# Kernel tuning notes

Hardware: AMD Instinct MI355X
Metric: run time of the kernel (lower is better)

The kernel has to match this reference:

```python
import jax, jax.numpy as jnp
import numpy as np

DIM = 128
B, LQ, LK = 8, 2048, 2048


def setup_inputs() -> dict:
    key = jax.random.key(0)
    k1, k2, k3 = jax.random.split(key, 3)
    output = jax.random.normal(k1, (B, LQ, DIM), dtype=jnp.float32)
    context = jax.random.normal(k2, (B, LK, DIM), dtype=jnp.float32)
    mask = jax.random.randint(k3, (B, LQ, LK), 0, 2).astype(jnp.bool_)
    return {"output": output, "context": context, "mask": mask}


def reference(output, context, mask):
    temperature = jnp.asarray(np.power(DIM, 0.5), dtype=output.dtype)
    # scores: [B, Lq, Lk]
    attn = jnp.einsum('bqd,bkd->bqk', output, context) / temperature
    attn = jnp.where(mask, -jnp.inf, attn)
    out_attn = jax.nn.log_softmax(attn, axis=-1)
    p = jax.nn.softmax(attn, axis=-1)
    # dropout is identity in eval/reference mode
    out = jnp.einsum('bqk,bkd->bqd', p, context)
    return (out, out_attn)
```

## Files before the change

### kernel.cpp

```cpp
#include <hip/hip_runtime.h>
#include <cstdint>


#define DIMV 128
constexpr int BB = 8;
constexpr int LQ = 2048;
constexpr int LK = 2048;
constexpr float QSCALE = 0.08838834764831843f;

typedef _Float16 half8 __attribute__((ext_vector_type(8)));
typedef _Float16 half4v __attribute__((ext_vector_type(4)));
typedef float float4v __attribute__((ext_vector_type(4)));

__global__ __launch_bounds__(256) void prep_kernel(const float* __restrict__ q,
                                                   const float* __restrict__ ctx,
                                                   _Float16* __restrict__ Qf,
                                                   _Float16* __restrict__ Kf,
                                                   _Float16* __restrict__ Vf) {
    __shared__ float tile[32][132];
    const int tid  = threadIdx.x;
    const int mode = blockIdx.x >> 9;
    const int t    = blockIdx.x & 511;
    const int b    = t >> 6;
    const int r0   = (t & 63) * 32;
    const float4* s4 = (const float4*)((mode == 0 ? q : ctx) + ((size_t)b * 2048 + r0) * DIMV);
    for (int v = 0; v < 4; v++) {
        int off = tid + v * 256;
        float4 f = s4[off];
        int row = off >> 5, c4 = (off & 31) * 4;
        tile[row][c4 + 0] = f.x; tile[row][c4 + 1] = f.y;
        tile[row][c4 + 2] = f.z; tile[row][c4 + 3] = f.w;
    }
    __syncthreads();
    if (mode < 2) {
        const float qs = (mode == 0) ? QSCALE : 1.0f;
        _Float16* dst = (mode == 0 ? Qf : Kf) + (size_t)b * (2048 * DIMV);
        for (int c = 0; c < 2; c++) {
            int chunk = tid + c * 256;
            int t2 = chunk >> 8, kk = (chunk >> 6) & 3, lane = chunk & 63;
            int quad = lane >> 4, l16 = lane & 15;
            int r = t2 * 16 + l16, d0 = kk * 32 + quad * 8;
            half8 h;
            for (int e = 0; e < 8; e++) h[e] = (_Float16)(tile[r][d0 + e] * qs);
            size_t tl = (size_t)(r0 >> 4) + t2;
            *(half8*)(dst + ((tl * 4 + kk) * 64 + lane) * 8) = h;
        }
    } else {
        _Float16* dst = Vf + (size_t)b * (2048 * DIMV);
        const int kt0 = r0 >> 4;
        for (int c = 0; c < 2; c++) {
            int chunk = tid + c * 256;
            int ktl = chunk >> 8, dp = (chunk >> 6) & 3, ln = chunk & 63;
            int qd = ln >> 4, s16 = ln & 15;
            half8 h;
            for (int e = 0; e < 4; e++) {
                h[e]     = (_Float16)tile[ktl * 16 + qd * 4 + e][(2 * dp) * 16 + s16];
                h[e + 4] = (_Float16)tile[ktl * 16 + qd * 4 + e][(2 * dp + 1) * 16 + s16];
            }
            *(half8*)(dst + ((((size_t)(kt0 + ktl)) * 4 + dp) * 64 + ln) * 8) = h;
        }
    }
}

__global__ __launch_bounds__(512, 1)
void attn_kernel(const unsigned char* __restrict__ mask,
                 const _Float16* __restrict__ Qf, const _Float16* __restrict__ Kf,
                 const _Float16* __restrict__ Vf,
                 float* __restrict__ out, float* __restrict__ out_attn) {
    __shared__ __attribute__((aligned(16))) _Float16 STG[2][16384];
    __shared__ __attribute__((aligned(16))) float pvsum[64][132];
    __shared__ float redm[8][32], redl[8][32], swf[8][32];
    __shared__ float mcl64[64], rls64[64];

    const int tid  = threadIdx.x;
    const int wave = tid >> 6;
    const int lane = tid & 63;
    const int l16  = lane & 15;
    const int quad = lane >> 4;
    const int p    = wave & 3;
    const int qg   = wave >> 2;

    const int b   = blockIdx.x & 7;
    const int qt4 = blockIdx.x >> 3;
    const int q0  = qt4 * 64;

    const _Float16* Qb = Qf + (size_t)b * (2048 * DIMV);
    const _Float16* Kb = Kf + (size_t)b * (2048 * DIMV);
    const _Float16* Vb = Vf + (size_t)b * (2048 * DIMV);

    half8 qfrag[2][4];
#pragma unroll
    for (int sub = 0; sub < 2; sub++) {
        const size_t tq = (size_t)qt4 * 4 + qg * 2 + sub;
#pragma unroll
        for (int kk = 0; kk < 4; kk++)
            qfrag[sub][kk] = *(const half8*)(Qb + ((tq * 4 + kk) * 64 + lane) * 8);
    }

    const unsigned char* mrow0 = mask + ((size_t)b * LQ + q0 + qg * 32 + l16) * LK + p * 16 + quad * 4;

    const float NEGINF = -__builtin_inff();
    float m0r = -1e30f, m1r = -1e30f;
    float l0r = 0.f, l1r = 0.f;
    float4v oacc[2][8];
#pragma unroll
    for (int sub = 0; sub < 2; sub++)
#pragma unroll
        for (int dt = 0; dt < 8; dt++) oacc[sub][dt] = (float4v){0.f, 0.f, 0.f, 0.f};

    const _Float16* gsb = (wave < 4) ? Kb : Vb;
    const int wt = wave & 3;
    const unsigned dsto = ((wave < 4) ? 0u : 8192u) + (unsigned)wt * 2048;

    {
        const _Float16* src = gsb + (size_t)(0 * 4 + wt) * 2048 + lane * 8;
        float4 r4[4];
#pragma unroll
        for (int c = 0; c < 4; c++) r4[c] = *(const float4*)(src + c * 512);
        _Float16* d = &STG[0][dsto];
#pragma unroll
        for (int c = 0; c < 4; c++) *(float4*)(d + c * 512 + lane * 8) = r4[c];
    }
    __syncthreads();

    for (int i = 0; i < 32; ++i) {
        const int cur = i & 1, nxt = cur ^ 1;
        const bool more = (i + 1 < 32);
        float4 nr4[4];
        if (more) {
            const _Float16* src = gsb + (size_t)(4 * (i + 1) + wt) * 2048 + lane * 8;
#pragma unroll
            for (int c = 0; c < 4; c++) nr4[c] = *(const float4*)(src + c * 512);
        }

        const _Float16* kt = &STG[cur][p * 2048];
        const _Float16* vt = &STG[cur][8192 + p * 2048];
        half8 kf[4], vv[4];
#pragma unroll
        for (int kk = 0; kk < 4; kk++) kf[kk] = *(const half8*)(kt + kk * 512 + lane * 8);
#pragma unroll
        for (int dp = 0; dp < 4; dp++) vv[dp] = *(const half8*)(vt + dp * 512 + lane * 8);

#pragma unroll
        for (int sub = 0; sub < 2; sub++) {
            float4v st = (float4v){0.f, 0.f, 0.f, 0.f};
#pragma unroll
            for (int kk = 0; kk < 4; kk++)
                st = __builtin_amdgcn_mfma_f32_16x16x32_f16(kf[kk], qfrag[sub][kk], st, 0, 0, 0);
            const uint32_t mv = *(const uint32_t*)(mrow0 + (size_t)sub * 16 * LK + (size_t)i * 64);
            float& m = sub ? m1r : m0r;
            float& l = sub ? l1r : l0r;
            float sv[4];
#pragma unroll
            for (int r = 0; r < 4; r++) {
                float v = st[r];
                if ((mv >> (8 * r)) & 0xffu) v = NEGINF;
                sv[r] = v;
            }
            float tmax = fmaxf(fmaxf(sv[0], sv[1]), fmaxf(sv[2], sv[3]));
            tmax = fmaxf(tmax, __shfl_xor(tmax, 16));
            tmax = fmaxf(tmax, __shfl_xor(tmax, 32));
            const bool upd = tmax > m + 3.0f;
            if (__any(upd)) {
                const float mnew = upd ? tmax : m;
                const float sc = __expf(m - mnew);
                float scr[4];
#pragma unroll
                for (int r = 0; r < 4; r++) scr[r] = __shfl(sc, quad * 4 + r);
                l *= sc;
#pragma unroll
                for (int dt = 0; dt < 8; dt++)
#pragma unroll
                    for (int r = 0; r < 4; r++) oacc[sub][dt][r] *= scr[r];
                m = mnew;
            }
            half4v pa;
            float psum = 0.f;
#pragma unroll
            for (int r = 0; r < 4; r++) {
                const float pp = __expf(sv[r] - m);
                psum += pp;
                pa[r] = (_Float16)pp;
            }
            psum += __shfl_xor(psum, 16);
            psum += __shfl_xor(psum, 32);
            l += psum;
#pragma unroll
            for (int dp = 0; dp < 4; dp++) {
                half4v vlo = __builtin_shufflevector(vv[dp], vv[dp], 0, 1, 2, 3);
                half4v vhi = __builtin_shufflevector(vv[dp], vv[dp], 4, 5, 6, 7);
                oacc[sub][2 * dp]     = __builtin_amdgcn_mfma_f32_16x16x16f16(pa, vlo, oacc[sub][2 * dp],     0, 0, 0);
                oacc[sub][2 * dp + 1] = __builtin_amdgcn_mfma_f32_16x16x16f16(pa, vhi, oacc[sub][2 * dp + 1], 0, 0, 0);
            }
        }

        if (more) {
            _Float16* d = &STG[nxt][dsto];
#pragma unroll
            for (int c = 0; c < 4; c++) *(float4*)(d + c * 512 + lane * 8) = nr4[c];
        }
        __syncthreads();
    }

    if (quad == 0) {
        redm[wave][l16]      = m0r;  redm[wave][16 + l16] = m1r;
        redl[wave][l16]      = l0r;  redl[wave][16 + l16] = l1r;
    }
    float4 pre2[2];
    {
        const int t0 = wave >> 2, kkw = wave & 3;
        pre2[0] = *(const float4*)(Kb + (size_t)(t0)     * 2048 + kkw * 512 + lane * 8);
        pre2[1] = *(const float4*)(Kb + (size_t)(t0 + 2) * 2048 + kkw * 512 + lane * 8);
    }
    __syncthreads();
    if (tid < 64) {
        const int qg2 = tid >> 5, r32 = tid & 31;
        float mm[4], ll[4];
#pragma unroll
        for (int pp = 0; pp < 4; pp++) { mm[pp] = redm[qg2 * 4 + pp][r32]; ll[pp] = redl[qg2 * 4 + pp][r32]; }
        const float M = fmaxf(fmaxf(mm[0], mm[1]), fmaxf(mm[2], mm[3]));
        float L = 0.f;
#pragma unroll
        for (int pp = 0; pp < 4; pp++) {
            const float e = __expf(mm[pp] - M);
            swf[qg2 * 4 + pp][r32] = e;
            L += e * ll[pp];
        }
        mcl64[tid] = M + __logf(L);
        rls64[tid] = 1.0f / L;
    }
    __syncthreads();

    for (int rnd = 0; rnd < 4; ++rnd) {
        if (p == rnd) {
#pragma unroll
            for (int sub = 0; sub < 2; sub++)
#pragma unroll
                for (int r = 0; r < 4; r++) {
                    const int row = qg * 32 + sub * 16 + quad * 4 + r;
                    const float sc = swf[wave][sub * 16 + quad * 4 + r];
#pragma unroll
                    for (int dt = 0; dt < 8; dt++) {
                        const float v = oacc[sub][dt][r] * sc;
                        if (rnd == 0) pvsum[row][dt * 16 + l16] = v;
                        else          pvsum[row][dt * 16 + l16] += v;
                    }
                }
        }
        __syncthreads();
    }

    {
        const int row = tid >> 3;
        const int c0  = (tid & 7) * 16;
        const float rcl = rls64[row];
        float* op = out + ((size_t)b * LQ + q0 + row) * DIMV + c0;
#pragma unroll
        for (int h = 0; h < 4; h++) {
            float4v a = *(const float4v*)&pvsum[row][c0 + h * 4];
            float4v v;
#pragma unroll
            for (int j = 0; j < 4; j++) v[j] = a[j] * rcl;
            *(float4v*)(op + h * 4) = v;
        }
    }

    {
        const int t0 = wave >> 2, kkw = wave & 3;
        *(float4*)(&STG[0][(t0)     * 2048 + kkw * 512] + lane * 8) = pre2[0];
        *(float4*)(&STG[0][(t0 + 2) * 2048 + kkw * 512] + lane * 8) = pre2[1];
    }
    __syncthreads();

    const float mc0 = mcl64[qg * 32 + l16];
    const float mc1 = mcl64[qg * 32 + 16 + l16];
    float* oa0 = out_attn + ((size_t)b * LQ + q0 + qg * 32 + l16) * LK + p * 16 + quad * 4;
    for (int i = 0; i < 32; ++i) {
        const int cur = i & 1, nxt = cur ^ 1;
        const bool more = (i + 1 < 32);
        float4 n2[2];
        if (more) {
            const int t0 = wave >> 2, kkw = wave & 3;
            n2[0] = *(const float4*)(Kb + (size_t)(4 * (i + 1) + t0)     * 2048 + kkw * 512 + lane * 8);
            n2[1] = *(const float4*)(Kb + (size_t)(4 * (i + 1) + t0 + 2) * 2048 + kkw * 512 + lane * 8);
        }
        const _Float16* kt = &STG[cur][p * 2048];
        half8 kf[4];
#pragma unroll
        for (int kk = 0; kk < 4; kk++) kf[kk] = *(const half8*)(kt + kk * 512 + lane * 8);
#pragma unroll
        for (int sub = 0; sub < 2; sub++) {
            float4v st = (float4v){0.f, 0.f, 0.f, 0.f};
#pragma unroll
            for (int kk = 0; kk < 4; kk++)
                st = __builtin_amdgcn_mfma_f32_16x16x32_f16(kf[kk], qfrag[sub][kk], st, 0, 0, 0);
            const uint32_t mv = *(const uint32_t*)(mrow0 + (size_t)sub * 16 * LK + (size_t)i * 64);
            const float mc = sub ? mc1 : mc0;
            float4v o;
#pragma unroll
            for (int r = 0; r < 4; r++) {
                float lp = st[r] - mc;
                if ((mv >> (8 * r)) & 0xffu) lp = -1.0e30f;
                o[r] = fmaxf(lp, -1.0e30f);
            }
            *(float4v*)(oa0 + (size_t)sub * 16 * LK + (size_t)i * 64) = o;
        }
        if (more) {
            const int t0 = wave >> 2, kkw = wave & 3;
            *(float4*)(&STG[nxt][(t0)     * 2048 + kkw * 512] + lane * 8) = n2[0];
            *(float4*)(&STG[nxt][(t0 + 2) * 2048 + kkw * 512] + lane * 8) = n2[1];
        }
        __syncthreads();
    }
}

extern "C" void kernel_launch(void* const* d_in, const int* in_sizes, int n_in,
                              void* d_out, int out_size, void* d_ws, size_t ws_size,
                              hipStream_t stream) {
    const float* q_f32 = (const float*)d_in[0];
    const float* c_f32 = (const float*)d_in[1];
    const unsigned char* mask = (const unsigned char*)d_in[2];

    float* out      = (float*)d_out;
    float* out_attn = out + (size_t)BB * LQ * DIMV;

    _Float16* Qf = (_Float16*)d_ws;
    _Float16* Kf = Qf + (size_t)BB * LQ * DIMV;
    _Float16* Vf = Kf + (size_t)BB * LK * DIMV;

    prep_kernel<<<1536, 256, 0, stream>>>(q_f32, c_f32, Qf, Kf, Vf);
    attn_kernel<<<BB * (LQ / 64), 512, 0, stream>>>(mask, Qf, Kf, Vf, out, out_attn);
}
```

Baseline: 304.0 us.

## Drop LDS staging; each wave streams its own key strip into registers

The attention kernel moves from 512-thread blocks of 64 queries to 256-thread blocks of 32 queries. Each wave now owns a contiguous quarter of the keys and loads its K/V fragments and mask words straight from global memory into double-buffered registers, so the shared-memory staging buffers and the per-iteration __syncthreads are gone. MFMA sections are wrapped in s_setprio and a sched_barrier, and the row-sum reduction is moved after the PV MFMAs. The intent is to remove barrier stalls and LDS traffic and to allow two blocks per CU. In exchange, K/V are read from global or L2 by more blocks, and register pressure rises.

```diff
diff --git a/kernel.cpp b/kernel.cpp
--- a/kernel.cpp
+++ b/kernel.cpp
@@ -62,27 +62,24 @@
     }
 }
 
-__global__ __launch_bounds__(512, 1)
+__global__ __launch_bounds__(256, 2)
 void attn_kernel(const unsigned char* __restrict__ mask,
                  const _Float16* __restrict__ Qf, const _Float16* __restrict__ Kf,
                  const _Float16* __restrict__ Vf,
                  float* __restrict__ out, float* __restrict__ out_attn) {
-    __shared__ __attribute__((aligned(16))) _Float16 STG[2][16384];
-    __shared__ __attribute__((aligned(16))) float pvsum[64][132];
-    __shared__ float redm[8][32], redl[8][32], swf[8][32];
-    __shared__ float mcl64[64], rls64[64];
+    __shared__ __attribute__((aligned(16))) float pvsum[32][132];
+    __shared__ float redm[4][32], redl[4][32], swf[4][32];
+    __shared__ float mcl32[32], rls32[32];
 
     const int tid  = threadIdx.x;
     const int wave = tid >> 6;
     const int lane = tid & 63;
     const int l16  = lane & 15;
     const int quad = lane >> 4;
-    const int p    = wave & 3;
-    const int qg   = wave >> 2;
-
-    const int b   = blockIdx.x & 7;
-    const int qt4 = blockIdx.x >> 3;
-    const int q0  = qt4 * 64;
+
+    const int b  = blockIdx.x & 7;
+    const int qg = blockIdx.x >> 3;
+    const int q0 = qg * 32;
 
     const _Float16* Qb = Qf + (size_t)b * (2048 * DIMV);
     const _Float16* Kb = Kf + (size_t)b * (2048 * DIMV);
@@ -91,13 +88,16 @@
     half8 qfrag[2][4];
 #pragma unroll
     for (int sub = 0; sub < 2; sub++) {
-        const size_t tq = (size_t)qt4 * 4 + qg * 2 + sub;
+        const size_t tq = (size_t)qg * 2 + sub;
 #pragma unroll
         for (int kk = 0; kk < 4; kk++)
             qfrag[sub][kk] = *(const half8*)(Qb + ((tq * 4 + kk) * 64 + lane) * 8);
     }
 
-    const unsigned char* mrow0 = mask + ((size_t)b * LQ + q0 + qg * 32 + l16) * LK + p * 16 + quad * 4;
+    const unsigned char* mrow0 = mask + ((size_t)b * LQ + q0 + l16) * LK + wave * 512 + quad * 4;
+
+    const _Float16* kstrip = Kb + (size_t)wave * 32 * 2048;
+    const _Float16* vstrip = Vb + (size_t)wave * 32 * 2048;
 
     const float NEGINF = -__builtin_inff();
     float m0r = -1e30f, m1r = -1e30f;
@@ -108,46 +108,43 @@
 #pragma unroll
         for (int dt = 0; dt < 8; dt++) oacc[sub][dt] = (float4v){0.f, 0.f, 0.f, 0.f};
 
-    const _Float16* gsb = (wave < 4) ? Kb : Vb;
-    const int wt = wave & 3;
-    const unsigned dsto = ((wave < 4) ? 0u : 8192u) + (unsigned)wt * 2048;
-
+    half8 kfb[2][4], vvb[2][4];
+    uint32_t mvb[2][2];
     {
-        const _Float16* src = gsb + (size_t)(0 * 4 + wt) * 2048 + lane * 8;
-        float4 r4[4];
-#pragma unroll
-        for (int c = 0; c < 4; c++) r4[c] = *(const float4*)(src + c * 512);
-        _Float16* d = &STG[0][dsto];
-#pragma unroll
-        for (int c = 0; c < 4; c++) *(float4*)(d + c * 512 + lane * 8) = r4[c];
-    }
-    __syncthreads();
-
-    for (int i = 0; i < 32; ++i) {
-        const int cur = i & 1, nxt = cur ^ 1;
-        const bool more = (i + 1 < 32);
-        float4 nr4[4];
-        if (more) {
-            const _Float16* src = gsb + (size_t)(4 * (i + 1) + wt) * 2048 + lane * 8;
-#pragma unroll
-            for (int c = 0; c < 4; c++) nr4[c] = *(const float4*)(src + c * 512);
-        }
-
-        const _Float16* kt = &STG[cur][p * 2048];
-        const _Float16* vt = &STG[cur][8192 + p * 2048];
-        half8 kf[4], vv[4];
-#pragma unroll
-        for (int kk = 0; kk < 4; kk++) kf[kk] = *(const half8*)(kt + kk * 512 + lane * 8);
-#pragma unroll
-        for (int dp = 0; dp < 4; dp++) vv[dp] = *(const half8*)(vt + dp * 512 + lane * 8);
+#pragma unroll
+        for (int kk = 0; kk < 4; kk++) kfb[0][kk] = *(const half8*)(kstrip + (kk * 64 + lane) * 8);
+#pragma unroll
+        for (int dp = 0; dp < 4; dp++) vvb[0][dp] = *(const half8*)(vstrip + (dp * 64 + lane) * 8);
+#pragma unroll
+        for (int s = 0; s < 2; s++) mvb[0][s] = *(const uint32_t*)(mrow0 + (size_t)s * 16 * LK);
+    }
+
+#pragma unroll 2
+    for (int ct = 0; ct < 32; ++ct) {
+        const int cur = ct & 1, nxt = cur ^ 1;
+        const int cn  = (ct + 1) & 31;
+        {
+            const _Float16* kp = kstrip + (size_t)cn * 2048;
+            const _Float16* vp = vstrip + (size_t)cn * 2048;
+#pragma unroll
+            for (int kk = 0; kk < 4; kk++) kfb[nxt][kk] = *(const half8*)(kp + (kk * 64 + lane) * 8);
+#pragma unroll
+            for (int dp = 0; dp < 4; dp++) vvb[nxt][dp] = *(const half8*)(vp + (dp * 64 + lane) * 8);
+#pragma unroll
+            for (int s = 0; s < 2; s++)
+                mvb[nxt][s] = *(const uint32_t*)(mrow0 + (size_t)s * 16 * LK + cn * 16);
+        }
+        __builtin_amdgcn_sched_barrier(0);
 
 #pragma unroll
         for (int sub = 0; sub < 2; sub++) {
             float4v st = (float4v){0.f, 0.f, 0.f, 0.f};
+            __builtin_amdgcn_s_setprio(1);
 #pragma unroll
             for (int kk = 0; kk < 4; kk++)
-                st = __builtin_amdgcn_mfma_f32_16x16x32_f16(kf[kk], qfrag[sub][kk], st, 0, 0, 0);
-            const uint32_t mv = *(const uint32_t*)(mrow0 + (size_t)sub * 16 * LK + (size_t)i * 64);
+                st = __builtin_amdgcn_mfma_f32_16x16x32_f16(kfb[cur][kk], qfrag[sub][kk], st, 0, 0, 0);
+            __builtin_amdgcn_s_setprio(0);
+            const uint32_t mv = mvb[cur][sub];
             float& m = sub ? m1r : m0r;
             float& l = sub ? l1r : l0r;
             float sv[4];
@@ -175,70 +172,64 @@
                 m = mnew;
             }
             half4v pa;
-            float psum = 0.f;
+            float pp[4];
 #pragma unroll
             for (int r = 0; r < 4; r++) {
-                const float pp = __expf(sv[r] - m);
-                psum += pp;
-                pa[r] = (_Float16)pp;
-            }
+                pp[r] = __expf(sv[r] - m);
+                pa[r] = (_Float16)pp[r];
+            }
+            __builtin_amdgcn_s_setprio(1);
+#pragma unroll
+            for (int dp = 0; dp < 4; dp++) {
+                half4v vlo = __builtin_shufflevector(vvb[cur][dp], vvb[cur][dp], 0, 1, 2, 3);
+                half4v vhi = __builtin_shufflevector(vvb[cur][dp], vvb[cur][dp], 4, 5, 6, 7);
+                oacc[sub][2 * dp]     = __builtin_amdgcn_mfma_f32_16x16x16f16(pa, vlo, oacc[sub][2 * dp],     0, 0, 0);
+                oacc[sub][2 * dp + 1] = __builtin_amdgcn_mfma_f32_16x16x16f16(pa, vhi, oacc[sub][2 * dp + 1], 0, 0, 0);
+            }
+            __builtin_amdgcn_s_setprio(0);
+            float psum = (pp[0] + pp[1]) + (pp[2] + pp[3]);
             psum += __shfl_xor(psum, 16);
             psum += __shfl_xor(psum, 32);
             l += psum;
-#pragma unroll
-            for (int dp = 0; dp < 4; dp++) {
-                half4v vlo = __builtin_shufflevector(vv[dp], vv[dp], 0, 1, 2, 3);
-                half4v vhi = __builtin_shufflevector(vv[dp], vv[dp], 4, 5, 6, 7);
-                oacc[sub][2 * dp]     = __builtin_amdgcn_mfma_f32_16x16x16f16(pa, vlo, oacc[sub][2 * dp],     0, 0, 0);
-                oacc[sub][2 * dp + 1] = __builtin_amdgcn_mfma_f32_16x16x16f16(pa, vhi, oacc[sub][2 * dp + 1], 0, 0, 0);
-            }
-        }
-
-        if (more) {
-            _Float16* d = &STG[nxt][dsto];
-#pragma unroll
-            for (int c = 0; c < 4; c++) *(float4*)(d + c * 512 + lane * 8) = nr4[c];
-        }
-        __syncthreads();
+        }
     }
 
     if (quad == 0) {
         redm[wave][l16]      = m0r;  redm[wave][16 + l16] = m1r;
         redl[wave][l16]      = l0r;  redl[wave][16 + l16] = l1r;
     }
-    float4 pre2[2];
-    {
-        const int t0 = wave >> 2, kkw = wave & 3;
-        pre2[0] = *(const float4*)(Kb + (size_t)(t0)     * 2048 + kkw * 512 + lane * 8);
-        pre2[1] = *(const float4*)(Kb + (size_t)(t0 + 2) * 2048 + kkw * 512 + lane * 8);
-    }
+    half8 kf2[2][4];
+    uint32_t mv2[2][2];
+#pragma unroll
+    for (int kk = 0; kk < 4; kk++) kf2[0][kk] = *(const half8*)(kstrip + (kk * 64 + lane) * 8);
+#pragma unroll
+    for (int s = 0; s < 2; s++) mv2[0][s] = *(const uint32_t*)(mrow0 + (size_t)s * 16 * LK);
     __syncthreads();
-    if (tid < 64) {
-        const int qg2 = tid >> 5, r32 = tid & 31;
+    if (tid < 32) {
         float mm[4], ll[4];
 #pragma unroll
-        for (int pp = 0; pp < 4; pp++) { mm[pp] = redm[qg2 * 4 + pp][r32]; ll[pp] = redl[qg2 * 4 + pp][r32]; }
+        for (int p = 0; p < 4; p++) { mm[p] = redm[p][tid]; ll[p] = redl[p][tid]; }
         const float M = fmaxf(fmaxf(mm[0], mm[1]), fmaxf(mm[2], mm[3]));
         float L = 0.f;
 #pragma unroll
-        for (int pp = 0; pp < 4; pp++) {
-            const float e = __expf(mm[pp] - M);
-            swf[qg2 * 4 + pp][r32] = e;
-            L += e * ll[pp];
-        }
-        mcl64[tid] = M + __logf(L);
-        rls64[tid] = 1.0f / L;
+        for (int p = 0; p < 4; p++) {
+            const float e = __expf(mm[p] - M);
+            swf[p][tid] = e;
+            L += e * ll[p];
+        }
+        mcl32[tid] = M + __logf(L);
+        rls32[tid] = 1.0f / L;
     }
     __syncthreads();
 
     for (int rnd = 0; rnd < 4; ++rnd) {
-        if (p == rnd) {
+        if (wave == rnd) {
 #pragma unroll
             for (int sub = 0; sub < 2; sub++)
 #pragma unroll
                 for (int r = 0; r < 4; r++) {
-                    const int row = qg * 32 + sub * 16 + quad * 4 + r;
-                    const float sc = swf[wave][sub * 16 + quad * 4 + r];
+                    const int row = sub * 16 + quad * 4 + r;
+                    const float sc = swf[wave][row];
 #pragma unroll
                     for (int dt = 0; dt < 8; dt++) {
                         const float v = oacc[sub][dt][r] * sc;
@@ -253,7 +244,7 @@
     {
         const int row = tid >> 3;
         const int c0  = (tid & 7) * 16;
-        const float rcl = rls64[row];
+        const float rcl = rls32[row];
         float* op = out + ((size_t)b * LQ + q0 + row) * DIMV + c0;
 #pragma unroll
         for (int h = 0; h < 4; h++) {
@@ -265,36 +256,32 @@
         }
     }
 
-    {
-        const int t0 = wave >> 2, kkw = wave & 3;
-        *(float4*)(&STG[0][(t0)     * 2048 + kkw * 512] + lane * 8) = pre2[0];
-        *(float4*)(&STG[0][(t0 + 2) * 2048 + kkw * 512] + lane * 8) = pre2[1];
-    }
-    __syncthreads();
-
-    const float mc0 = mcl64[qg * 32 + l16];
-    const float mc1 = mcl64[qg * 32 + 16 + l16];
-    float* oa0 = out_attn + ((size_t)b * LQ + q0 + qg * 32 + l16) * LK + p * 16 + quad * 4;
-    for (int i = 0; i < 32; ++i) {
-        const int cur = i & 1, nxt = cur ^ 1;
-        const bool more = (i + 1 < 32);
-        float4 n2[2];
-        if (more) {
-            const int t0 = wave >> 2, kkw = wave & 3;
-            n2[0] = *(const float4*)(Kb + (size_t)(4 * (i + 1) + t0)     * 2048 + kkw * 512 + lane * 8);
-            n2[1] = *(const float4*)(Kb + (size_t)(4 * (i + 1) + t0 + 2) * 2048 + kkw * 512 + lane * 8);
-        }
-        const _Float16* kt = &STG[cur][p * 2048];
-        half8 kf[4];
-#pragma unroll
-        for (int kk = 0; kk < 4; kk++) kf[kk] = *(const half8*)(kt + kk * 512 + lane * 8);
+    const float mc0 = mcl32[l16];
+    const float mc1 = mcl32[16 + l16];
+    float* oa0 = out_attn + ((size_t)b * LQ + q0 + l16) * LK + wave * 512 + quad * 4;
+#pragma unroll 2
+    for (int ct = 0; ct < 32; ++ct) {
+        const int cur = ct & 1, nxt = cur ^ 1;
+        const int cn  = (ct + 1) & 31;
+        {
+            const _Float16* kp = kstrip + (size_t)cn * 2048;
+#pragma unroll
+            for (int kk = 0; kk < 4; kk++) kf2[nxt][kk] = *(const half8*)(kp + (kk * 64 + lane) * 8);
+#pragma unroll
+            for (int s = 0; s < 2; s++)
+                mv2[nxt][s] = *(const uint32_t*)(mrow0 + (size_t)s * 16 * LK + cn * 16);
+        }
+        __builtin_amdgcn_sched_barrier(0);
+
 #pragma unroll
         for (int sub = 0; sub < 2; sub++) {
             float4v st = (float4v){0.f, 0.f, 0.f, 0.f};
+            __builtin_amdgcn_s_setprio(1);
 #pragma unroll
             for (int kk = 0; kk < 4; kk++)
-                st = __builtin_amdgcn_mfma_f32_16x16x32_f16(kf[kk], qfrag[sub][kk], st, 0, 0, 0);
-            const uint32_t mv = *(const uint32_t*)(mrow0 + (size_t)sub * 16 * LK + (size_t)i * 64);
+                st = __builtin_amdgcn_mfma_f32_16x16x32_f16(kf2[cur][kk], qfrag[sub][kk], st, 0, 0, 0);
+            __builtin_amdgcn_s_setprio(0);
+            const uint32_t mv = mv2[cur][sub];
             const float mc = sub ? mc1 : mc0;
             float4v o;
 #pragma unroll
@@ -303,14 +290,8 @@
                 if ((mv >> (8 * r)) & 0xffu) lp = -1.0e30f;
                 o[r] = fmaxf(lp, -1.0e30f);
             }
-            *(float4v*)(oa0 + (size_t)sub * 16 * LK + (size_t)i * 64) = o;
-        }
-        if (more) {
-            const int t0 = wave >> 2, kkw = wave & 3;
-            *(float4*)(&STG[nxt][(t0)     * 2048 + kkw * 512] + lane * 8) = n2[0];
-            *(float4*)(&STG[nxt][(t0 + 2) * 2048 + kkw * 512] + lane * 8) = n2[1];
-        }
-        __syncthreads();
+            *(float4v*)(oa0 + (size_t)sub * 16 * LK + ct * 16) = o;
+        }
     }
 }
 
@@ -329,5 +310,5 @@
     _Float16* Vf = Kf + (size_t)BB * LK * DIMV;
 
     prep_kernel<<<1536, 256, 0, stream>>>(q_f32, c_f32, Qf, Kf, Vf);
-    attn_kernel<<<BB * (LQ / 64), 512, 0, stream>>>(mask, Qf, Kf, Vf, out, out_attn);
+    attn_kernel<<<BB * (LQ / 32), 256, 0, stream>>>(mask, Qf, Kf, Vf, out, out_attn);
 }
```

After: 277.1 us. -8.9%, faster.
